# Performance work log

Hardware: AMD Instinct MI355X
Metric: run time of the kernel (lower is better)

## Reference

```python
import jax, jax.numpy as jnp
import numpy as np

FEATURE_MAPS = [8, 4, 2, 1]
BOXES_PER_LOC = [4, 6, 6, 4]
IMAGE_SIZE = 128
DECODED_SIZE = 64
Z_WHAT = 64
CHANNELS = [64, 256, 128, 64, 32, 16, 3]  # conv-transpose pyramid 1x1 -> 64x64
BATCH = 4
EMPTY_CONST = -1000.0
N_LOC = sum(f * f for f in FEATURE_MAPS)            # 85
N_BOX = sum(f * f * b for f, b in zip(FEATURE_MAPS, BOXES_PER_LOC))  # 380


def _recon_indices():
    # Decoder.reconstruction_indices: expand per-location latents to per-box.
    idx, last = [], 0
    for fm, bpl in zip(FEATURE_MAPS, BOXES_PER_LOC):
        for i in range(fm * fm):
            idx.append(np.full(bpl, last + i, dtype=np.int32))
        last += fm * fm
    return np.concatenate(idx)


def setup_inputs() -> dict:
    key = jax.random.key(0)
    ks = jax.random.split(key, 16)
    inp = {
        'z_what': jax.random.normal(ks[0], (BATCH, N_LOC, Z_WHAT), jnp.float32),
        'z_where': jax.random.uniform(ks[1], (BATCH, N_BOX, 4), jnp.float32),
        'z_present': jax.random.randint(ks[2], (BATCH, N_BOX, 1), 0, 2).astype(jnp.int32),
        'z_depth': jax.random.normal(ks[3], (BATCH, N_LOC, 1), jnp.float32),
    }
    for i, (cin, cout) in enumerate(zip(CHANNELS[:-1], CHANNELS[1:])):
        inp[f'w{i}'] = jax.random.normal(ks[4 + i], (2, 2, cin, cout), jnp.float32) / np.sqrt(4.0 * cin)
        inp[f'b{i}'] = jnp.zeros((cout,), jnp.float32)
    return inp


def _what_decoder(z_flat, params):
    # (N, Z) -> (N, 3, 64, 64): stack of stride-2 kernel-2 conv transposes.
    x = z_flat[:, :, None, None]
    n = len(params)
    for i, (w, b) in enumerate(params):
        x = jax.lax.conv_transpose(x, w, strides=(2, 2), padding='VALID',
                                   dimension_numbers=('NCHW', 'HWIO', 'NCHW'))
        x = x + b[None, :, None, None]
        x = jax.nn.sigmoid(x) if i == n - 1 else jax.nn.relu(x)
    return x


def _sample_bilinear(img, px, py):
    # img (3, D, D); px/py (S,) pixel coords along cols/rows; zero outside.
    D = DECODED_SIZE
    x0 = jnp.floor(px)
    y0 = jnp.floor(py)
    wx = px - x0
    wy = py - y0

    def gather(yi, xi):
        vy = (yi >= 0) & (yi <= D - 1)
        vx = (xi >= 0) & (xi <= D - 1)
        yc = jnp.clip(yi.astype(jnp.int32), 0, D - 1)
        xc = jnp.clip(xi.astype(jnp.int32), 0, D - 1)
        vals = img[:, yc[:, None], xc[None, :]]  # (3, S, S)
        return vals * (vy[:, None] & vx[None, :]).astype(img.dtype)

    g00 = gather(y0, x0)
    g01 = gather(y0, x0 + 1)
    g10 = gather(y0 + 1, x0)
    g11 = gather(y0 + 1, x0 + 1)
    wyc = wy[None, :, None]
    wxc = wx[None, None, :]
    return (g00 * (1 - wyc) * (1 - wxc) + g01 * (1 - wyc) * wxc
            + g10 * wyc * (1 - wxc) + g11 * wyc * wxc)


def _where_stn(imgs, z_where):
    # Paste each decoded glyph into an IMAGE_SIZE canvas at box (cx, cy, w, h).
    S, D = IMAGE_SIZE, DECODED_SIZE
    cx, cy, w, h = (z_where[:, i] for i in range(4))
    sx = jnp.maximum(w, 1e-5)
    sy = jnp.maximum(h, 1e-5)
    out = jnp.linspace(-1.0, 1.0, S)
    xin = (out[None, :] - (2 * cx - 1)[:, None]) / sx[:, None]  # (N, S)
    yin = (out[None, :] - (2 * cy - 1)[:, None]) / sy[:, None]
    px = (xin + 1) * (D - 1) / 2
    py = (yin + 1) * (D - 1) / 2
    return jax.vmap(_sample_bilinear)(imgs, px, py)  # (N, 3, S, S)


def reference(z_what, z_where, z_present, z_depth, w0, b0, w1, b1, w2, b2, w3, b3, w4, b4, w5, b5):
    params = [(w0, b0), (w1, b1), (w2, b2), (w3, b3), (w4, b4), (w5, b5)]
    idx = jnp.asarray(_recon_indices())
    zw = jnp.take(z_what, idx, axis=1)   # (B, N_BOX, Z)
    zd = jnp.take(z_depth, idx, axis=1)  # (B, N_BOX, 1)
    B = zw.shape[0]
    decoded = _what_decoder(zw.reshape(B * N_BOX, Z_WHAT), params)
    transformed = _where_stn(decoded, z_where.reshape(B * N_BOX, 4))
    recon = transformed.reshape(B, N_BOX, 3, IMAGE_SIZE, IMAGE_SIZE)
    depths = jnp.where(z_present[..., 0] == 1, zd[..., 0], EMPTY_CONST)  # (B, N_BOX)
    weights = jax.nn.softmax(depths, axis=1)
    return jnp.einsum('bn,bnchw->bchw', weights, recon)
```

## Files before the change

### kernel.cpp

```cpp
#include <hip/hip_runtime.h>
#include <hip/hip_bf16.h>

#define NBOX  380
#define NLOCS 85
#define NINST 340

__device__ __forceinline__ int loc_of_box(int n) {
    if (n < 256) return n >> 2;
    if (n < 352) return 64 + (n - 256) / 6;
    if (n < 376) return 80 + (n - 352) / 6;
    return 84;
}

__device__ void box_params_dev(int b, const float* __restrict__ zwhere,
    const int* __restrict__ zpresent, const float* __restrict__ zdepth,
    float* wgt, float* sxs, float* oxs, float* sys, float* oys,
    int* binst, int* rect, int* cidx, int* cnt, float* sm)
{
    float* sd  = sm;
    float* red = sm + 384;
    const int tid = threadIdx.x;

    if (tid < NBOX) {
        int loc = loc_of_box(tid);
        sd[tid] = (zpresent[b * NBOX + tid] == 1) ? zdepth[b * NLOCS + loc] : -1000.0f;
    }
    __syncthreads();

    float m = (tid < NBOX) ? sd[tid] : -1e30f;
    red[tid] = m; __syncthreads();
    for (int s = 256; s > 0; s >>= 1) {
        if (tid < s) red[tid] = fmaxf(red[tid], red[tid + s]);
        __syncthreads();
    }
    m = red[0]; __syncthreads();

    float sum = (tid < NBOX) ? expf(sd[tid] - m) : 0.f;
    red[tid] = sum; __syncthreads();
    for (int s = 256; s > 0; s >>= 1) {
        if (tid < s) red[tid] += red[tid + s];
        __syncthreads();
    }
    float inv = 1.0f / red[0];
    __syncthreads();

    if (tid < NBOX) {
        int g = b * NBOX + tid;
        float wv = expf(sd[tid] - m) * inv;
        wgt[g] = wv;
        float cx = zwhere[g * 4 + 0], cy = zwhere[g * 4 + 1];
        float w  = zwhere[g * 4 + 2], h  = zwhere[g * 4 + 3];
        float isx = 1.0f / fmaxf(w, 1e-5f);
        float isy = 1.0f / fmaxf(h, 1e-5f);
        float sxv = isx * (63.0f / 127.0f);
        float oxv = 31.5f * (1.0f - 2.0f * cx * isx);
        float syv = isy * (63.0f / 127.0f);
        float oyv = 31.5f * (1.0f - 2.0f * cy * isy);
        sxs[g] = sxv; oxs[g] = oxv; sys[g] = syv; oys[g] = oyv;
        binst[g] = b * NLOCS + loc_of_box(tid);
        int wlo = min(127, max(0, (int)floorf((-1.0f - oxv) / sxv)));
        int whi = max(0, min(127, (int)ceilf((64.0f - oxv) / sxv)));
        int hlo = min(127, max(0, (int)floorf((-1.0f - oyv) / syv)));
        int hhi = max(0, min(127, (int)ceilf((64.0f - oyv) / syv)));
        rect[g] = wlo | (whi << 8) | (hlo << 16) | (hhi << 24);
        sd[tid] = wv;
    }
    __syncthreads();

    if (tid < 64) {
        int base = 0;
        for (int c = 0; c < 6; ++c) {
            int n = c * 64 + tid;
            bool p = (n < NBOX) && (sd[n] > 0.0f);
            unsigned long long mask = __ballot(p);
            int pos = __popcll(mask & ((1ull << tid) - 1ull));
            if (p) cidx[b * NBOX + base + pos] = n;
            base += __popcll(mask);
        }
        if (tid == 0) cnt[b] = base;
    }
}

__global__ __launch_bounds__(512, 2) void decode_fused_k(
    const float* __restrict__ z_what,
    const float* __restrict__ W0, const float* __restrict__ B0,
    const float* __restrict__ W1, const float* __restrict__ B1,
    const float* __restrict__ W2, const float* __restrict__ B2,
    const float* __restrict__ W3, const float* __restrict__ B3,
    const float* __restrict__ W4, const float* __restrict__ B4,
    const float* __restrict__ W5, const float* __restrict__ B5,
    const float* __restrict__ z_where, const int* __restrict__ z_present,
    const float* __restrict__ z_depth,
    float* __restrict__ wgt, float* __restrict__ sxs, float* __restrict__ oxs,
    float* __restrict__ sys, float* __restrict__ oys, int* __restrict__ binst,
    int* __restrict__ rect, int* __restrict__ cidx, int* __restrict__ cnt,
    float* __restrict__ dec)
{
    __shared__ __align__(16) float sm[12416];

    if (blockIdx.x >= NINST) {
        box_params_dev(blockIdx.x - NINST, z_where, z_present, z_depth,
                       wgt, sxs, oxs, sys, oys, binst, rect, cidx, cnt, sm);
        return;
    }

    float* L2o = sm;
    float* s_x = sm + 4224;
    float* L0o = sm + 4288;
    float* L1o = sm + 5312;
    float* L3o = sm + 4224;
    float* L4b = sm;

    const int inst = blockIdx.x;
    const int tid = threadIdx.x;
    const int lane = tid & 63;
    const int wv = __builtin_amdgcn_readfirstlane(tid >> 6);

    if (tid < 64) s_x[tid] = z_what[inst * 64 + tid];
    __syncthreads();

    {
        const int co = tid & 255;
        const int tg = __builtin_amdgcn_readfirstlane(tid >> 8);
        const float* wA = W0 + (size_t)(3 - tg) * 64 * 256 + co;
        const float* wB = W0 + (size_t)(1 - tg) * 64 * 256 + co;
        float a0 = 0.f, a1 = 0.f;
        #pragma unroll 8
        for (int k = 0; k < 64; ++k) {
            float xv = s_x[k];
            a0 = fmaf(xv, wA[k * 256], a0);
            a1 = fmaf(xv, wB[k * 256], a1);
        }
        float bb = B0[co];
        L0o[tg * 256 + co]       = fmaxf(a0 + bb, 0.f);
        L0o[(tg + 2) * 256 + co] = fmaxf(a1 + bb, 0.f);
    }
    __syncthreads();

    {
        const int co = tid & 127;
        const int t = __builtin_amdgcn_readfirstlane(tid >> 7);
        const int ft = 3 - t, di = t >> 1, dj = t & 1;
        const float* wp = W1 + (size_t)ft * 256 * 128 + co;
        float acc[4] = {0.f, 0.f, 0.f, 0.f};
        #pragma unroll 2
        for (int q = 0; q < 64; ++q) {
            int k0 = q * 4;
            float4 x0 = *(const float4*)&L0o[0 * 256 + k0];
            float4 x1 = *(const float4*)&L0o[1 * 256 + k0];
            float4 x2 = *(const float4*)&L0o[2 * 256 + k0];
            float4 x3 = *(const float4*)&L0o[3 * 256 + k0];
            float w0 = wp[(k0 + 0) * 128], w1 = wp[(k0 + 1) * 128];
            float w2 = wp[(k0 + 2) * 128], w3 = wp[(k0 + 3) * 128];
            acc[0] = fmaf(x0.x, w0, acc[0]); acc[0] = fmaf(x0.y, w1, acc[0]);
            acc[0] = fmaf(x0.z, w2, acc[0]); acc[0] = fmaf(x0.w, w3, acc[0]);
            acc[1] = fmaf(x1.x, w0, acc[1]); acc[1] = fmaf(x1.y, w1, acc[1]);
            acc[1] = fmaf(x1.z, w2, acc[1]); acc[1] = fmaf(x1.w, w3, acc[1]);
            acc[2] = fmaf(x2.x, w0, acc[2]); acc[2] = fmaf(x2.y, w1, acc[2]);
            acc[2] = fmaf(x2.z, w2, acc[2]); acc[2] = fmaf(x2.w, w3, acc[2]);
            acc[3] = fmaf(x3.x, w0, acc[3]); acc[3] = fmaf(x3.y, w1, acc[3]);
            acc[3] = fmaf(x3.z, w2, acc[3]); acc[3] = fmaf(x3.w, w3, acc[3]);
        }
        float bb = B1[co];
        #pragma unroll
        for (int p = 0; p < 4; ++p) {
            int i = p >> 1, j = p & 1;
            L1o[((2 * i + di) * 4 + 2 * j + dj) * 128 + co] = fmaxf(acc[p] + bb, 0.f);
        }
    }
    __syncthreads();

    {
        const int co = lane;
        const int t = wv & 3, ih = wv >> 2;
        const int ft = 3 - t, di = t >> 1, dj = t & 1;
        const float* wp = W2 + (size_t)ft * 128 * 64 + co;
        float acc[8] = {0.f,0.f,0.f,0.f,0.f,0.f,0.f,0.f};
        #pragma unroll 2
        for (int q = 0; q < 32; ++q) {
            int k0 = q * 4;
            float w0 = wp[(k0 + 0) * 64], w1 = wp[(k0 + 1) * 64];
            float w2 = wp[(k0 + 2) * 64], w3 = wp[(k0 + 3) * 64];
            #pragma unroll
            for (int pp = 0; pp < 8; ++pp) {
                float4 xq = *(const float4*)&L1o[(ih * 8 + pp) * 128 + k0];
                acc[pp] = fmaf(xq.x, w0, acc[pp]);
                acc[pp] = fmaf(xq.y, w1, acc[pp]);
                acc[pp] = fmaf(xq.z, w2, acc[pp]);
                acc[pp] = fmaf(xq.w, w3, acc[pp]);
            }
        }
        float bb = B2[co];
        #pragma unroll
        for (int pp = 0; pp < 8; ++pp) {
            int p = ih * 8 + pp;
            int i = p >> 2, j = p & 3;
            int op = (2 * i + di) * 8 + 2 * j + dj;
            L2o[co * 66 + op] = fmaxf(acc[pp] + bb, 0.f);
        }
    }
    __syncthreads();

    {
        const int di = wv >> 2, coq = wv & 3;
        const int ft0 = 3 - 2 * di, ft1 = 2 - 2 * di;
        const float* w0b = W3 + (size_t)ft0 * 64 * 32 + coq * 8;
        const float* w1b = W3 + (size_t)ft1 * 64 * 32 + coq * 8;
        float a0[8], a1[8];
        #pragma unroll
        for (int c = 0; c < 8; ++c) { a0[c] = 0.f; a1[c] = 0.f; }
        #pragma unroll 4
        for (int k = 0; k < 64; ++k) {
            float xv = L2o[k * 66 + lane];
            const float* w0p = w0b + k * 32;
            const float* w1p = w1b + k * 32;
            #pragma unroll
            for (int c = 0; c < 8; ++c) {
                a0[c] = fmaf(xv, w0p[c], a0[c]);
                a1[c] = fmaf(xv, w1p[c], a1[c]);
            }
        }
        int i = lane >> 3, j = lane & 7;
        #pragma unroll
        for (int c = 0; c < 8; ++c) {
            float bb = B3[coq * 8 + c];
            float2 v = make_float2(fmaxf(a0[c] + bb, 0.f), fmaxf(a1[c] + bb, 0.f));
            *(float2*)&L3o[(coq * 8 + c) * 256 + (2 * i + di) * 16 + 2 * j] = v;
        }
    }
    __syncthreads();

    const int t5 = wv & 3, pxh5 = wv >> 2;
    const int ft5 = 3 - t5, di5 = t5 >> 1, dj5 = t5 & 1;
    float w5r[16][3];
    #pragma unroll
    for (int k = 0; k < 16; ++k)
        #pragma unroll
        for (int c = 0; c < 3; ++c)
            w5r[k][c] = W5[(ft5 * 16 + k) * 3 + c];
    const float b50 = B5[0], b51 = B5[1], b52 = B5[2];

    for (int c4 = 0; c4 < 4; ++c4) {
        {
            const int di4 = wv >> 2, coq4 = wv & 3;
            const int ft0 = 3 - 2 * di4, ft1 = 2 - 2 * di4;
            const float* w0b = W4 + (size_t)ft0 * 32 * 16 + coq4 * 4;
            const float* w1b = W4 + (size_t)ft1 * 32 * 16 + coq4 * 4;
            float a0[4], a1[4];
            #pragma unroll
            for (int c = 0; c < 4; ++c) { a0[c] = 0.f; a1[c] = 0.f; }
            #pragma unroll 4
            for (int k = 0; k < 32; ++k) {
                float xv = L3o[k * 256 + 64 * c4 + lane];
                const float* w0p = w0b + k * 16;
                const float* w1p = w1b + k * 16;
                #pragma unroll
                for (int c = 0; c < 4; ++c) {
                    a0[c] = fmaf(xv, w0p[c], a0[c]);
                    a1[c] = fmaf(xv, w1p[c], a1[c]);
                }
            }
            int il = lane >> 4, j = lane & 15;
            #pragma unroll
            for (int c = 0; c < 4; ++c) {
                float bb = B4[coq4 * 4 + c];
                float2 v = make_float2(fmaxf(a0[c] + bb, 0.f), fmaxf(a1[c] + bb, 0.f));
                *(float2*)&L4b[(coq4 * 4 + c) * 258 + (2 * il + di4) * 32 + 2 * j] = v;
            }
        }
        __syncthreads();
        {
            #pragma unroll
            for (int sub = 0; sub < 2; ++sub) {
                int pl = pxh5 * 128 + sub * 64 + lane;
                int r = pl >> 5, x5 = pl & 31;
                int y5 = 8 * c4 + r;
                float a0 = b50, a1 = b51, a2 = b52;
                #pragma unroll
                for (int k = 0; k < 16; ++k) {
                    float xv = L4b[k * 258 + pl];
                    a0 = fmaf(xv, w5r[k][0], a0);
                    a1 = fmaf(xv, w5r[k][1], a1);
                    a2 = fmaf(xv, w5r[k][2], a2);
                }
                a0 = 1.0f / (1.0f + expf(-a0));
                a1 = 1.0f / (1.0f + expf(-a1));
                a2 = 1.0f / (1.0f + expf(-a2));
                float* dp = dec + (size_t)inst * 16384
                          + (size_t)((2 * y5 + di5) * 64 + 2 * x5 + dj5) * 4;
                *(float4*)dp = make_float4(a0, a1, a2, 0.f);
            }
        }
        __syncthreads();
    }
}

__global__ __launch_bounds__(1024) void composite_k(
    const float* __restrict__ dec, const float* __restrict__ wgt,
    const float* __restrict__ sxs, const float* __restrict__ oxs,
    const float* __restrict__ sys, const float* __restrict__ oys,
    const int* __restrict__ binst, const int* __restrict__ rect,
    const int* __restrict__ cidx, const int* __restrict__ cnt,
    float* __restrict__ out)
{
    __shared__ float pls[8][128][3];

    int b = blockIdx.x >> 7, tile = blockIdx.x & 127;
    int tx0 = (tile & 7) << 4, ty0 = (tile >> 3) << 3;
    int s = threadIdx.x >> 7, px = threadIdx.x & 127;
    int lx = px & 15, ly = px >> 4;
    int w = tx0 + lx, h = ty0 + ly;

    int nb = cnt[b];
    int lo = (nb * s) >> 3, hi = (nb * (s + 1)) >> 3;

    float fw = (float)w, fh = (float)h;
    float a0 = 0.f, a1 = 0.f, a2 = 0.f;
    for (int q = lo; q < hi; ++q) {
        int n = cidx[b * NBOX + q];
        int rc = rect[b * NBOX + n];
        int wlo = rc & 255, whi = (rc >> 8) & 255;
        int hlo = (rc >> 16) & 255, hhi = (rc >> 24) & 255;
        if (whi < tx0 || wlo > tx0 + 15 || hhi < ty0 || hlo > ty0 + 7) continue;
        int g = b * NBOX + n;
        float wg = wgt[g];
        float pxx = fmaf(fw, sxs[g], oxs[g]);
        float pyy = fmaf(fh, sys[g], oys[g]);
        float x0 = floorf(pxx), y0 = floorf(pyy);
        if (x0 < -1.0f || x0 > 63.0f || y0 < -1.0f || y0 > 63.0f) continue;
        float wx = pxx - x0, wy = pyy - y0;
        int ix = (int)x0, iy = (int)y0;
        int x0c = max(ix, 0), x1c = min(ix + 1, 63);
        int y0c = max(iy, 0), y1c = min(iy + 1, 63);
        float m00 = (ix >= 0 && iy >= 0) ? 1.f : 0.f;
        float m01 = (ix + 1 <= 63 && iy >= 0) ? 1.f : 0.f;
        float m10 = (ix >= 0 && iy + 1 <= 63) ? 1.f : 0.f;
        float m11 = (ix + 1 <= 63 && iy + 1 <= 63) ? 1.f : 0.f;
        float w00 = (1.f - wy) * (1.f - wx) * m00;
        float w01 = (1.f - wy) * wx * m01;
        float w10 = wy * (1.f - wx) * m10;
        float w11 = wy * wx * m11;
        const float* img = dec + (size_t)binst[g] * 16384;
        float4 v00 = *(const float4*)&img[(y0c * 64 + x0c) * 4];
        float4 v01 = *(const float4*)&img[(y0c * 64 + x1c) * 4];
        float4 v10 = *(const float4*)&img[(y1c * 64 + x0c) * 4];
        float4 v11 = *(const float4*)&img[(y1c * 64 + x1c) * 4];
        a0 += wg * (w00 * v00.x + w01 * v01.x + w10 * v10.x + w11 * v11.x);
        a1 += wg * (w00 * v00.y + w01 * v01.y + w10 * v10.y + w11 * v11.y);
        a2 += wg * (w00 * v00.z + w01 * v01.z + w10 * v10.z + w11 * v11.z);
    }
    pls[s][px][0] = a0; pls[s][px][1] = a1; pls[s][px][2] = a2;
    __syncthreads();

    if (threadIdx.x < 384) {
        int c = threadIdx.x >> 7, p2 = threadIdx.x & 127;
        float v = 0.f;
        #pragma unroll
        for (int t = 0; t < 8; ++t) v += pls[t][p2][c];
        int h2 = ty0 + (p2 >> 4), w2 = tx0 + (p2 & 15);
        out[((b * 3 + c) * 128 + h2) * 128 + w2] = v;
    }
}

extern "C" void kernel_launch(void* const* d_in, const int* in_sizes, int n_in,
                              void* d_out, int out_size, void* d_ws, size_t ws_size,
                              hipStream_t stream)
{
    const float* z_what    = (const float*)d_in[0];
    const float* z_where   = (const float*)d_in[1];
    const int*   z_present = (const int*)  d_in[2];
    const float* z_depth   = (const float*)d_in[3];

    char* ws = (char*)d_ws;
    float* dec = (float*)ws;
    float* P   = (float*)(ws + 22282240);
    float* wgt = P,        *sxs = P + 1520, *oxs = P + 2 * 1520;
    float* sys = P + 3 * 1520, *oys = P + 4 * 1520;
    int* binst = (int*)(P + 5 * 1520);
    int* rect  = binst + 1520;
    int* cidx  = binst + 2 * 1520;
    int* cnt   = binst + 3 * 1520;

    decode_fused_k<<<dim3(NINST + 4), dim3(512), 0, stream>>>(
        z_what,
        (const float*)d_in[4],  (const float*)d_in[5],
        (const float*)d_in[6],  (const float*)d_in[7],
        (const float*)d_in[8],  (const float*)d_in[9],
        (const float*)d_in[10], (const float*)d_in[11],
        (const float*)d_in[12], (const float*)d_in[13],
        (const float*)d_in[14], (const float*)d_in[15],
        z_where, z_present, z_depth,
        wgt, sxs, oxs, sys, oys, binst, rect, cidx, cnt,
        dec);

    composite_k<<<dim3(512), dim3(1024), 0, stream>>>(
        dec, wgt, sxs, oxs, sys, oys, binst, rect, cidx, cnt, (float*)d_out);
}
```

Measured before the change: 87.67 us.

## Retile conv-transpose layers 1 and 2 with register-blocked output channels and pixels

Layers 1 and 2 of the fused decoder are rethreaded so that each thread computes a small 2-pixel by 2- or 4-channel tile. Weights are loaded as float2/float4 vectors and reused across two pixels, and activations are reused across channels. Previously each thread did one channel over 4 or 8 pixels with scalar weight loads. The L1o row stride is padded from 128 to 132, presumably to reduce LDS bank conflicts. This is meant to cut global weight load instructions and LDS traffic per FMA, at the cost of different per-thread load patterns and possibly more LDS reads per FMA in layer 2.

New measurement: 109.4 us. +24.8%, slower.

```diff
diff --git a/kernel.cpp b/kernel.cpp
--- a/kernel.cpp
+++ b/kernel.cpp
@@ -10,6 +10,10 @@
     if (n < 352) return 64 + (n - 256) / 6;
     if (n < 376) return 80 + (n - 352) / 6;
     return 84;
+}
+
+__device__ __forceinline__ float f4e(const float4& v, int kk) {
+    return (kk == 0) ? v.x : (kk == 1) ? v.y : (kk == 2) ? v.z : v.w;
 }
 
 __device__ void box_params_dev(int b, const float* __restrict__ zwhere,
@@ -138,65 +142,70 @@
     __syncthreads();
 
     {
-        const int co = tid & 127;
-        const int t = __builtin_amdgcn_readfirstlane(tid >> 7);
+        const int co2 = tid & 63;
+        const int wv1 = tid >> 6;
+        const int pxp = wv1 & 1;
+        const int t   = wv1 >> 1;
         const int ft = 3 - t, di = t >> 1, dj = t & 1;
-        const float* wp = W1 + (size_t)ft * 256 * 128 + co;
-        float acc[4] = {0.f, 0.f, 0.f, 0.f};
-        #pragma unroll 2
+        const float* wp = W1 + (size_t)ft * 256 * 128 + co2 * 2;
+        const float* xp0 = L0o + (2 * pxp + 0) * 256;
+        const float* xp1 = L0o + (2 * pxp + 1) * 256;
+        float a00 = 0.f, a01 = 0.f, a10 = 0.f, a11 = 0.f;
+        #pragma unroll 4
         for (int q = 0; q < 64; ++q) {
             int k0 = q * 4;
-            float4 x0 = *(const float4*)&L0o[0 * 256 + k0];
-            float4 x1 = *(const float4*)&L0o[1 * 256 + k0];
-            float4 x2 = *(const float4*)&L0o[2 * 256 + k0];
-            float4 x3 = *(const float4*)&L0o[3 * 256 + k0];
-            float w0 = wp[(k0 + 0) * 128], w1 = wp[(k0 + 1) * 128];
-            float w2 = wp[(k0 + 2) * 128], w3 = wp[(k0 + 3) * 128];
-            acc[0] = fmaf(x0.x, w0, acc[0]); acc[0] = fmaf(x0.y, w1, acc[0]);
-            acc[0] = fmaf(x0.z, w2, acc[0]); acc[0] = fmaf(x0.w, w3, acc[0]);
-            acc[1] = fmaf(x1.x, w0, acc[1]); acc[1] = fmaf(x1.y, w1, acc[1]);
-            acc[1] = fmaf(x1.z, w2, acc[1]); acc[1] = fmaf(x1.w, w3, acc[1]);
-            acc[2] = fmaf(x2.x, w0, acc[2]); acc[2] = fmaf(x2.y, w1, acc[2]);
-            acc[2] = fmaf(x2.z, w2, acc[2]); acc[2] = fmaf(x2.w, w3, acc[2]);
-            acc[3] = fmaf(x3.x, w0, acc[3]); acc[3] = fmaf(x3.y, w1, acc[3]);
-            acc[3] = fmaf(x3.z, w2, acc[3]); acc[3] = fmaf(x3.w, w3, acc[3]);
-        }
-        float bb = B1[co];
-        #pragma unroll
-        for (int p = 0; p < 4; ++p) {
-            int i = p >> 1, j = p & 1;
-            L1o[((2 * i + di) * 4 + 2 * j + dj) * 128 + co] = fmaxf(acc[p] + bb, 0.f);
-        }
+            float4 x0 = *(const float4*)&xp0[k0];
+            float4 x1 = *(const float4*)&xp1[k0];
+            #pragma unroll
+            for (int kk = 0; kk < 4; ++kk) {
+                float2 w2 = *(const float2*)&wp[(k0 + kk) * 128];
+                float e0 = f4e(x0, kk), e1 = f4e(x1, kk);
+                a00 = fmaf(e0, w2.x, a00); a01 = fmaf(e0, w2.y, a01);
+                a10 = fmaf(e1, w2.x, a10); a11 = fmaf(e1, w2.y, a11);
+            }
+        }
+        float2 b2 = *(const float2*)&B1[co2 * 2];
+        int p0 = 2 * pxp, p1 = p0 + 1;
+        int o0 = ((2 * (p0 >> 1) + di) * 4 + 2 * (p0 & 1) + dj) * 132 + co2 * 2;
+        int o1 = ((2 * (p1 >> 1) + di) * 4 + 2 * (p1 & 1) + dj) * 132 + co2 * 2;
+        *(float2*)&L1o[o0] = make_float2(fmaxf(a00 + b2.x, 0.f), fmaxf(a01 + b2.y, 0.f));
+        *(float2*)&L1o[o1] = make_float2(fmaxf(a10 + b2.x, 0.f), fmaxf(a11 + b2.y, 0.f));
     }
     __syncthreads();
 
     {
-        const int co = lane;
-        const int t = wv & 3, ih = wv >> 2;
+        const int co4 = tid & 15;
+        const int g   = (tid >> 4) & 7;
+        const int t   = tid >> 7;
         const int ft = 3 - t, di = t >> 1, dj = t & 1;
-        const float* wp = W2 + (size_t)ft * 128 * 64 + co;
-        float acc[8] = {0.f,0.f,0.f,0.f,0.f,0.f,0.f,0.f};
-        #pragma unroll 2
+        const float* wp = W2 + (size_t)ft * 128 * 64 + co4 * 4;
+        const float* xp0 = L1o + (2 * g + 0) * 132;
+        const float* xp1 = L1o + (2 * g + 1) * 132;
+        float aP[4] = {0.f,0.f,0.f,0.f}, aQ[4] = {0.f,0.f,0.f,0.f};
+        #pragma unroll 4
         for (int q = 0; q < 32; ++q) {
             int k0 = q * 4;
-            float w0 = wp[(k0 + 0) * 64], w1 = wp[(k0 + 1) * 64];
-            float w2 = wp[(k0 + 2) * 64], w3 = wp[(k0 + 3) * 64];
-            #pragma unroll
-            for (int pp = 0; pp < 8; ++pp) {
-                float4 xq = *(const float4*)&L1o[(ih * 8 + pp) * 128 + k0];
-                acc[pp] = fmaf(xq.x, w0, acc[pp]);
-                acc[pp] = fmaf(xq.y, w1, acc[pp]);
-                acc[pp] = fmaf(xq.z, w2, acc[pp]);
-                acc[pp] = fmaf(xq.w, w3, acc[pp]);
-            }
-        }
-        float bb = B2[co];
+            float4 x0 = *(const float4*)&xp0[k0];
+            float4 x1 = *(const float4*)&xp1[k0];
+            #pragma unroll
+            for (int kk = 0; kk < 4; ++kk) {
+                float4 w4 = *(const float4*)&wp[(k0 + kk) * 64];
+                float e0 = f4e(x0, kk), e1 = f4e(x1, kk);
+                aP[0] = fmaf(e0, w4.x, aP[0]); aP[1] = fmaf(e0, w4.y, aP[1]);
+                aP[2] = fmaf(e0, w4.z, aP[2]); aP[3] = fmaf(e0, w4.w, aP[3]);
+                aQ[0] = fmaf(e1, w4.x, aQ[0]); aQ[1] = fmaf(e1, w4.y, aQ[1]);
+                aQ[2] = fmaf(e1, w4.z, aQ[2]); aQ[3] = fmaf(e1, w4.w, aQ[3]);
+            }
+        }
+        float4 b4 = *(const float4*)&B2[co4 * 4];
+        float bb[4] = {b4.x, b4.y, b4.z, b4.w};
+        int p0 = 2 * g, p1 = p0 + 1;
+        int op0 = (2 * (p0 >> 2) + di) * 8 + 2 * (p0 & 3) + dj;
+        int op1 = (2 * (p1 >> 2) + di) * 8 + 2 * (p1 & 3) + dj;
         #pragma unroll
-        for (int pp = 0; pp < 8; ++pp) {
-            int p = ih * 8 + pp;
-            int i = p >> 2, j = p & 3;
-            int op = (2 * i + di) * 8 + 2 * j + dj;
-            L2o[co * 66 + op] = fmaxf(acc[pp] + bb, 0.f);
+        for (int c = 0; c < 4; ++c) {
+            L2o[(co4 * 4 + c) * 66 + op0] = fmaxf(aP[c] + bb[c], 0.f);
+            L2o[(co4 * 4 + c) * 66 + op1] = fmaxf(aQ[c] + bb[c], 0.f);
         }
     }
     __syncthreads();
```
